# Optimization experiments

Measured on AMD Instinct MI355X. Metric: run time of the kernel, lower is better.

## Reference

```python
import jax, jax.numpy as jnp
import numpy as np
from jax import lax

# ---- config (matches DecodePredictions init kwargs) ----
MAX_PER_CLASS = 100
MAX_TOTAL = 100
IOU_THRESH = 0.5
SCORE_THRESH = 0.05
NUM_CLASSES = 80
K_CAND = 512  # per-class candidate pool kept before NMS (bounds the O(K^2) IoU work)
BOX_VARIANCE = np.array([0.1, 0.1, 0.2, 0.2], np.float32)


def generate_anchors(height, width):
    """RetinaNet anchors (keras.io AnchorBox): FPN levels 3-7, 3 ratios x 3 scales, [cx,cy,w,h] in pixels."""
    ratios = [0.5, 1.0, 2.0]
    scales = [2 ** 0.0, 2 ** (1.0 / 3.0), 2 ** (2.0 / 3.0)]
    all_anchors = []
    for level in range(3, 8):
        stride = 2 ** level
        area = float((2 ** (level + 2)) ** 2)  # 32^2 .. 512^2
        dims = []
        for r in ratios:
            ah = np.sqrt(area / r)
            aw = area / ah
            for s in scales:
                dims.append([s * aw, s * ah])
        dims = np.asarray(dims, np.float32)  # [9, 2] = (w, h)
        fh = int(np.ceil(height / stride))
        fw = int(np.ceil(width / stride))
        rx = (np.arange(fw, dtype=np.float32) + 0.5) * stride
        ry = (np.arange(fh, dtype=np.float32) + 0.5) * stride
        cx, cy = np.meshgrid(rx, ry)
        centers = np.stack([cx, cy], -1)[:, :, None, :].repeat(9, axis=2)  # [fh,fw,9,2]
        d = np.broadcast_to(dims, (fh, fw, 9, 2))
        all_anchors.append(np.concatenate([centers, d], -1).reshape(-1, 4).astype(np.float32))
    return jnp.asarray(np.concatenate(all_anchors, 0))  # [N, 4]


def _pairwise_iou(b):
    # Generic TF NMS IoU formula treating coords as [y1,x1,y2,x2] (module feeds cx,cy,w,h -- replicated faithfully).
    y1, x1, y2, x2 = b[:, 0], b[:, 1], b[:, 2], b[:, 3]
    area = jnp.maximum(y2 - y1, 0.0) * jnp.maximum(x2 - x1, 0.0)
    ih = jnp.maximum(jnp.minimum(y2[:, None], y2[None, :]) - jnp.maximum(y1[:, None], y1[None, :]), 0.0)
    iw = jnp.maximum(jnp.minimum(x2[:, None], x2[None, :]) - jnp.maximum(x1[:, None], x1[None, :]), 0.0)
    inter = ih * iw
    union = area[:, None] + area[None, :] - inter
    return jnp.where(union > 0.0, inter / union, 0.0)


def _nms_single_class(boxes, scores):  # boxes [N,4], scores [N]
    top_s, idx = lax.top_k(scores, K_CAND)          # sort-by-score candidate pool
    top_b = boxes[idx]                               # [K,4]
    keep0 = top_s > SCORE_THRESH                     # score_threshold filter
    iou = _pairwise_iou(top_b)                       # [K,K]
    rng = jnp.arange(K_CAND)

    def body(i, keep):
        sup = (iou[i] > IOU_THRESH) & (rng > i)      # boxes ranked below i suppressed by i
        return jnp.where(keep[i], keep & ~sup, keep)

    keep = lax.fori_loop(0, K_CAND, body, keep0)
    kept_s = jnp.where(keep, top_s, 0.0)
    sel_s, sel = lax.top_k(kept_s, MAX_PER_CLASS)    # max_output_size_per_class
    return top_b[sel], sel_s                         # [P,4], [P]


def _combine(cls_boxes, cls_scores):  # [C,P,4], [C,P] -> combined top MAX_TOTAL for one image
    C, P = cls_scores.shape
    flat_s = cls_scores.reshape(-1)
    flat_b = cls_boxes.reshape(-1, 4)
    flat_c = jnp.repeat(jnp.arange(C, dtype=jnp.float32), P)
    top_s, idx = lax.top_k(flat_s, MAX_TOTAL)
    valid = (top_s > 0.0)
    vf = valid.astype(flat_b.dtype)
    boxes = jnp.clip(flat_b[idx], 0.0, 1.0) * vf[:, None]  # clip_boxes=True, zero-pad invalid
    scores = top_s * vf
    classes = jnp.where(valid, flat_c[idx], 0.0)
    return boxes, scores, classes, valid.sum().astype(jnp.int32)


def _forward(inputs, predictions):
    H, W = inputs.shape[1], inputs.shape[2]
    anchors = generate_anchors(float(H), float(W))            # [N,4] cx,cy,w,h
    cls_scores = jax.nn.sigmoid(predictions[..., :-4])        # [B,N,C]
    box_pred = predictions[..., -4:] * jnp.asarray(BOX_VARIANCE)
    xy = box_pred[..., :2] * anchors[..., 2:] + anchors[..., :2]
    wh = jnp.exp(box_pred[..., 2:]) * anchors[..., 2:]
    boxes = jnp.concatenate([xy, wh], -1)                     # [B,N,4] decoded

    per_class = jax.vmap(jax.vmap(_nms_single_class, in_axes=(None, 1)), in_axes=(0, 0))
    cb, cs = per_class(boxes, cls_scores)                     # [B,C,P,4], [B,C,P]
    return jax.vmap(_combine)(cb, cs)                         # boxes, scores, classes, valid


def setup_inputs() -> dict:
    key = jax.random.key(0)
    k1, k2 = jax.random.split(key)
    inputs = jax.random.uniform(k1, (4, 640, 640, 3), jnp.float32)
    predictions = jax.random.normal(k2, (4, 76725, NUM_CLASSES + 4), jnp.float32)
    return {"inputs": inputs, "predictions": predictions}


def reference(inputs, predictions):
    return _forward(inputs, predictions)
```

## Files before the change

kernel.cpp:

```cpp
#include <hip/hip_runtime.h>
#include <cmath>

#define NA 76725
#define NCLS 80
#define NB 4
#define KC 512
#define MPC 100
#define MT 100
#define TT 256
#define NTILE 300
#define NSLOTP 300
#define PADN 76800
#define NCAND 1024
#define SLOT 16
#define SPLIT 8
#define THRESH_LOGIT 2.3f

struct Dims { float d[5 * 9 * 2]; };


__device__ __forceinline__ unsigned keyof(float x) {
    unsigned u = __float_as_uint(x);
    return u ^ ((u & 0x80000000u) ? 0xFFFFFFFFu : 0x80000000u);
}
__device__ __forceinline__ float unkey(unsigned k) {
    unsigned u = (k & 0x80000000u) ? (k ^ 0x80000000u) : ~k;
    return __uint_as_float(u);
}
__device__ __forceinline__ float sigmoidf_dev(float x) {
    if (x >= 0.f) return 1.f / (1.f + expf(-x));
    float e = expf(x);
    return e / (1.f + e);
}
__device__ __forceinline__ unsigned long long compose(unsigned key, int a) {
    return ((unsigned long long)key << 32) | (unsigned long long)(0xFFFFFFFFu - (unsigned)a);
}

__device__ __forceinline__ float4 decode_box(float4 p, int a, const Dims& dims) {
    const int base[5] = {0, 57600, 72000, 75600, 76500};
    const int fw[5] = {80, 40, 20, 10, 5};
    const float strd[5] = {8.f, 16.f, 32.f, 64.f, 128.f};
    int l;
    if (a < 57600) l = 0;
    else if (a < 72000) l = 1;
    else if (a < 75600) l = 2;
    else if (a < 76500) l = 3;
    else l = 4;
    int i = a - base[l];
    int cell = i / 9, k = i - cell * 9;
    int x = cell % fw[l], y = cell / fw[l];
    float cx = ((float)x + 0.5f) * strd[l];
    float cy = ((float)y + 0.5f) * strd[l];
    float aw = dims.d[(l * 9 + k) * 2 + 0];
    float ah = dims.d[(l * 9 + k) * 2 + 1];
    float bx = __fmul_rn(p.x, 0.1f), by = __fmul_rn(p.y, 0.1f);
    float bw = __fmul_rn(p.z, 0.2f), bh = __fmul_rn(p.w, 0.2f);
    float4 o;
    o.x = __fadd_rn(__fmul_rn(bx, aw), cx);
    o.y = __fadd_rn(__fmul_rn(by, ah), cy);
    o.z = __fmul_rn(expf(bw), aw);
    o.w = __fmul_rn(expf(bh), ah);
    return o;
}


__global__ __launch_bounds__(256) void scan_kernel(const float* __restrict__ pred,
                                                   unsigned long long* __restrict__ candbuf,
                                                   int* __restrict__ counts2) {
    __shared__ int cnt[NCLS];
    __shared__ unsigned long long hitbuf[NCLS * SLOT];
    const int blk = blockIdx.x;
    const int b = blk / NTILE, tix = blk - b * NTILE;
    const int t0 = tix * TT;
    int nrow = NA - t0; if (nrow > TT) nrow = TT;

    if (threadIdx.x < NCLS) cnt[threadIdx.x] = 0;
    __syncthreads();

    const float4* src = reinterpret_cast<const float4*>(pred + ((size_t)b * NA + t0) * 84);
    const int nv = nrow * 21;

    #define PROC(v, idx) do {                                                  \
        const int row_ = (idx) / 21, chunk_ = (idx) - row_ * 21;               \
        if (chunk_ != 20) {                                                    \
            const int a_ = t0 + row_, cbase_ = chunk_ * 4;                     \
            const float vals_[4] = {(v).x, (v).y, (v).z, (v).w};               \
            _Pragma("unroll")                                                  \
            for (int q_ = 0; q_ < 4; ++q_) {                                   \
                if (vals_[q_] > THRESH_LOGIT) {                                \
                    const int c_ = cbase_ + q_;                                \
                    const int p_ = atomicAdd(&cnt[c_], 1);                     \
                    if (p_ < SLOT)                                             \
                        hitbuf[c_ * SLOT + p_] = compose(keyof(vals_[q_]), a_);\
                }                                                              \
            }                                                                  \
        }                                                                      \
    } while (0)

    int i = threadIdx.x;
    for (; i + 768 < nv; i += 1024) {
        const float4 v0 = src[i];
        const float4 v1 = src[i + 256];
        const float4 v2 = src[i + 512];
        const float4 v3 = src[i + 768];
        PROC(v0, i); PROC(v1, i + 256); PROC(v2, i + 512); PROC(v3, i + 768);
    }
    for (; i < nv; i += 256) {
        const float4 v = src[i];
        PROC(v, i);
    }
    #undef PROC
    __syncthreads();

    for (int e = threadIdx.x; e < NCLS * SLOT; e += 256) {
        const int c = e >> 4, q = e & (SLOT - 1);
        if (q < cnt[c])
            candbuf[(((size_t)(b * NCLS + c)) * NSLOTP + tix) * SLOT + q] = hitbuf[e];
    }
    if (threadIdx.x < NCLS)
        counts2[(size_t)(b * NCLS + threadIdx.x) * NSLOTP + tix] = cnt[threadIdx.x];
}


__device__ __forceinline__ void find_bin(int* hist, int bins, int remaining,
                                         int* sh3, int* wsum) {
    const int tid = threadIdx.x;
    const int lane = tid & 63, wv = tid >> 6;
    const int nit = (bins + 511) >> 9;
    int lsum = 0;
    for (int q = 0; q < nit; ++q) {
        int rr = tid * nit + q;
        if (rr < bins) lsum += hist[bins - 1 - rr];
    }
    int acc = lsum;
    #pragma unroll
    for (int off = 1; off < 64; off <<= 1) {
        int x = __shfl_up(acc, off);
        if (lane >= off) acc += x;
    }
    if (lane == 63) wsum[wv] = acc;
    __syncthreads();
    int base = 0;
    for (int w = 0; w < wv; ++w) base += wsum[w];
    int run = base + acc - lsum;
    for (int q = 0; q < nit; ++q) {
        int rr = tid * nit + q;
        if (rr < bins) {
            int h = hist[bins - 1 - rr];
            if (run < remaining && remaining <= run + h) { sh3[0] = bins - 1 - rr; sh3[1] = run; sh3[2] = h; }
            run += h;
        }
    }
    __syncthreads();
}


__global__ __launch_bounds__(512) void topk2_kernel(const float* __restrict__ pred,
                                                    const unsigned long long* __restrict__ candbuf,
                                                    const int* __restrict__ counts2,
                                                    float* __restrict__ top_score,
                                                    float4* __restrict__ sel_boxes, Dims dims) {
    const int col = blockIdx.x;
    const int b = col / NCLS, cc = col - b * NCLS;
    const int tid = threadIdx.x;
    const int lane = tid & 63, wv = tid >> 6;

    __shared__ int hist4k[4096];
    __shared__ unsigned long long buf[KC];
    __shared__ int hist[256];
    __shared__ int sh3[3];
    __shared__ int wsum[8];
    __shared__ int gcount, eqtaken, totsh, ovfsh;
    __shared__ int wcnt[8];
    unsigned long long* cand = (unsigned long long*)hist4k;
    int* scnt = hist4k + 2048;
    int* spfx = hist4k + 2560;

    if (tid == 0) { totsh = 0; ovfsh = 0; }
    int lsum = (tid < NSLOTP) ? counts2[(size_t)col * NSLOTP + tid] : 0;
    scnt[tid] = lsum;
    if (lsum > SLOT) ovfsh = 1;
    int acc = lsum;
    #pragma unroll
    for (int off = 1; off < 64; off <<= 1) {
        int x = __shfl_up(acc, off);
        if (lane >= off) acc += x;
    }
    if (lane == 63) wsum[wv] = acc;
    __syncthreads();
    int base = 0;
    for (int w = 0; w < wv; ++w) base += wsum[w];
    spfx[tid] = base + acc - lsum;
    if (tid == 511) totsh = base + acc;
    __syncthreads();

    const int tot = totsh;
    const bool fastok = (!ovfsh) && tot >= KC && tot <= NCAND;
    int mode = 0;

    if (fastok) {
        cand[tid] = 0ull; cand[tid + 512] = 0ull;
        __syncthreads();
        const unsigned long long* src = candbuf + (size_t)col * NSLOTP * SLOT;
        for (int i = tid; i < NSLOTP * SLOT; i += 512) {
            const int e = i >> 4, q = i & (SLOT - 1);
            const unsigned long long v = src[i];
            if (q < scnt[e]) cand[spfx[e] + q] = v;
        }
        __syncthreads();
    } else {
        const float* colp = pred + (size_t)b * NA * 84 + cc;
        for (int i = tid; i < 4096; i += 512) hist4k[i] = 0;
        __syncthreads();
        for (int a = tid; a < NA; a += 512)
            atomicAdd(&hist4k[keyof(colp[(size_t)a * 84]) >> 20], 1);
        __syncthreads();
        find_bin(hist4k, 4096, KC, sh3, wsum);
        const int bsel = sh3[0], above = sh3[1], ceq1 = sh3[2];
        const int ncand = above + ceq1;

        if (ncand <= NCAND) {
            const unsigned fk = ((unsigned)bsel) << 20;
            if (tid == 0) gcount = 0;
            cand[tid] = 0ull; cand[tid + 512] = 0ull;
            __syncthreads();
            for (int a = tid; a < NA; a += 512) {
                unsigned k = keyof(colp[(size_t)a * 84]);
                if (k >= fk) { int p = atomicAdd(&gcount, 1); cand[p] = compose(k, a); }
            }
            __syncthreads();
        } else {
            mode = 1;
            unsigned prefix = ((unsigned)bsel) << 20;
            int remaining = KC - above;

            for (int i = tid; i < 4096; i += 512) hist4k[i] = 0;
            __syncthreads();
            for (int a = tid; a < NA; a += 512) {
                unsigned k = keyof(colp[(size_t)a * 84]);
                if ((k & 0xFFF00000u) == prefix) atomicAdd(&hist4k[(k >> 8) & 4095], 1);
            }
            __syncthreads();
            find_bin(hist4k, 4096, remaining, sh3, wsum);
            prefix |= ((unsigned)sh3[0]) << 8;
            remaining -= sh3[1];

            if (tid < 256) hist[tid] = 0;
            __syncthreads();
            for (int a = tid; a < NA; a += 512) {
                unsigned k = keyof(colp[(size_t)a * 84]);
                if ((k & 0xFFFFFF00u) == prefix) atomicAdd(&hist[k & 255], 1);
            }
            __syncthreads();
            find_bin(hist, 256, remaining, sh3, wsum);
            prefix |= (unsigned)sh3[0];
            remaining -= sh3[1];

            const unsigned K = prefix;
            const int cgt = KC - remaining;
            const int need = remaining;
            if (tid == 0) { gcount = 0; eqtaken = 0; }
            __syncthreads();
            for (int bs = 0; bs < PADN; bs += 512) {
                int a = bs + tid;
                unsigned key = (a < NA) ? keyof(colp[(size_t)a * 84]) : 0u;
                if (a < NA && key > K) {
                    int p = atomicAdd(&gcount, 1);
                    buf[p] = compose(key, a);
                }
                bool eq = (key == K) && (a < NA);
                unsigned long long m = __ballot(eq);
                if (lane == 0) wcnt[wv] = __popcll(m);
                __syncthreads();
                int off = eqtaken;
                for (int w = 0; w < wv; ++w) off += wcnt[w];
                int rank = off + __popcll(m & ((1ull << lane) - 1ull));
                if (eq && rank < need)
                    buf[cgt + rank] = compose(K, a);
                __syncthreads();
                if (tid == 0) {
                    int s = 0;
                    for (int w = 0; w < 8; ++w) s += wcnt[w];
                    eqtaken += s;
                }
                __syncthreads();
            }
        }
    }

    if (mode == 0) {
        for (int k2 = 2; k2 <= NCAND; k2 <<= 1) {
            for (int j = k2 >> 1; j > 0; j >>= 1) {
                __syncthreads();
                for (int i = tid; i < NCAND; i += 512) {
                    int ixj = i ^ j;
                    if (ixj > i) {
                        unsigned long long A = cand[i], B = cand[ixj];
                        bool up = (i & k2) == 0;
                        if (up ? (A < B) : (A > B)) { cand[i] = B; cand[ixj] = A; }
                    }
                }
            }
        }
    } else {
        for (int k2 = 2; k2 <= KC; k2 <<= 1) {
            for (int j = k2 >> 1; j > 0; j >>= 1) {
                __syncthreads();
                {
                    int i = tid, ixj = i ^ j;
                    if (ixj > i) {
                        unsigned long long A = buf[i], B = buf[ixj];
                        bool up = (i & k2) == 0;
                        if (up ? (A < B) : (A > B)) { buf[i] = B; buf[ixj] = A; }
                    }
                }
            }
        }
    }
    __syncthreads();

    {
        const unsigned long long v = (mode == 0) ? cand[tid] : buf[tid];
        const unsigned key = (unsigned)(v >> 32);
        const int a = (int)(0xFFFFFFFFu - (unsigned)(v & 0xFFFFFFFFu));
        top_score[col * KC + tid] = sigmoidf_dev(unkey(key));
        const float4 p4 = *reinterpret_cast<const float4*>(pred + ((size_t)b * NA + a) * 84 + 80);
        sel_boxes[(size_t)col * KC + tid] = decode_box(p4, a, dims);
    }
}


__global__ __launch_bounds__(512) void nms_build_kernel(const float4* __restrict__ sel_boxes,
                                                        unsigned long long* __restrict__ maskbuf) {
    const int blk = blockIdx.x;
    const int col = blk >> 3, part = blk & 7;
    const int tid = threadIdx.x, wave = tid >> 6, lane = tid & 63;
    __shared__ float y1[KC], x1[KC], y2[KC], x2[KC], ar[KC];

    for (int t = tid; t < KC; t += 512) {
        float4 bx = sel_boxes[(size_t)col * KC + t];
        y1[t] = bx.x; x1[t] = bx.y; y2[t] = bx.z; x2[t] = bx.w;
        ar[t] = __fmul_rn(fmaxf(__fsub_rn(bx.z, bx.x), 0.f),
                          fmaxf(__fsub_rn(bx.w, bx.y), 0.f));
    }
    __syncthreads();

    float jy1[8], jx1[8], jy2[8], jx2[8], jar[8];
    #pragma unroll
    for (int w = 0; w < 8; ++w) {
        int j = (w << 6) + lane;
        jy1[w] = y1[j]; jx1[w] = x1[j]; jy2[w] = y2[j]; jx2[w] = x2[j]; jar[w] = ar[j];
    }

    for (int k = 0; k < 8; ++k) {
        const int i = part + SPLIT * (wave + 8 * k);
        const float iy1 = y1[i], ix1 = x1[i], iy2 = y2[i], ix2 = x2[i], iar = ar[i];
        unsigned long long row[8];
        #pragma unroll
        for (int w = 0; w < 8; ++w) {
            unsigned long long m = 0ull;
            if (((w << 6) + 63) > i) {
                const int j = (w << 6) + lane;
                float ih = fmaxf(__fsub_rn(fminf(iy2, jy2[w]), fmaxf(iy1, jy1[w])), 0.f);
                float iw = fmaxf(__fsub_rn(fminf(ix2, jx2[w]), fmaxf(ix1, jx1[w])), 0.f);
                float inter = __fmul_rn(ih, iw);
                float uni = __fsub_rn(__fadd_rn(iar, jar[w]), inter);
                m = __ballot((uni > 0.f) && (inter > __fmul_rn(0.5f, uni)) && (j > i));
            }
            row[w] = m;
        }
        unsigned long long v = row[0];
        v = (lane == 1) ? row[1] : v;
        v = (lane == 2) ? row[2] : v;
        v = (lane == 3) ? row[3] : v;
        v = (lane == 4) ? row[4] : v;
        v = (lane == 5) ? row[5] : v;
        v = (lane == 6) ? row[6] : v;
        v = (lane == 7) ? row[7] : v;
        if (lane < 8) maskbuf[((size_t)col * KC + i) * 8 + lane] = v;
    }
}


__global__ __launch_bounds__(512) void nms_resolve_kernel(const float4* __restrict__ sel_boxes,
                                                          const float* __restrict__ top_score,
                                                          const unsigned long long* __restrict__ maskbuf,
                                                          float4* __restrict__ col_boxes,
                                                          float* __restrict__ col_scores) {
    const int col = blockIdx.x;
    const int tid = threadIdx.x, wv = tid >> 6, lane = tid & 63;
    __shared__ unsigned long long mask[KC * 8];
    __shared__ float y1[KC], x1[KC], y2[KC], x2[KC], sc[KC];
    __shared__ unsigned long long keep0w[8], keepw[8];
    __shared__ int wordpfx[9];
    __shared__ int sel[MPC];

    {
        const unsigned long long* src = maskbuf + (size_t)col * KC * 8;
        for (int m = tid; m < KC * 8; m += 512) mask[m] = src[m];
    }
    {
        const int t = tid;
        float4 bx = sel_boxes[(size_t)col * KC + t];
        y1[t] = bx.x; x1[t] = bx.y; y2[t] = bx.z; x2[t] = bx.w;
        const float s = top_score[col * KC + t];
        sc[t] = s;
        const unsigned long long m = __ballot(s > 0.05f);
        if (lane == 0) keep0w[t >> 6] = m;
    }
    __syncthreads();

    if (wv == 0) {
        const int w8 = lane & 7;
        const unsigned long long kww = keep0w[w8];
        unsigned long long remw = 0ull;
        for (int ib = 0; ib < KC; ib += 8) {
            unsigned long long rows[8];
            #pragma unroll
            for (int u = 0; u < 8; ++u) rows[u] = mask[(ib + u) * 8 + w8];
            #pragma unroll
            for (int u = 0; u < 8; ++u) {
                const int i = ib + u, W = i >> 6, t = i & 63;
                const unsigned long long remW = __shfl(remw, W);
                const unsigned long long kwW = __shfl(kww, W);
                if (((kwW >> t) & 1ull) && !((remW >> t) & 1ull)) remw |= rows[u];
            }
        }
        if (lane < 8) keepw[w8] = kww & ~remw;
    }
    __syncthreads();
    if (tid == 0) {
        int s = 0;
        #pragma unroll
        for (int w = 0; w < 8; ++w) { wordpfx[w] = s; s += __popcll(keepw[w]); }
        wordpfx[8] = s;
    }
    __syncthreads();

    const int nkept = wordpfx[8];
    {
        const int t = tid;
        const unsigned long long w = keepw[t >> 6];
        const int l = t & 63;
        const bool kp = (w >> l) & 1ull;
        const int kb = wordpfx[t >> 6] + __popcll(w & ((1ull << l) - 1ull));
        if (kp) {
            if (kb < MPC) sel[kb] = t;
        } else {
            const int nb = t - kb;
            if (nkept + nb < MPC) sel[nkept + nb] = t;
        }
    }
    __syncthreads();
    if (tid < MPC) {
        int t = sel[tid];
        bool kp = (keepw[t >> 6] >> (t & 63)) & 1ull;
        col_scores[col * MPC + tid] = kp ? sc[t] : 0.f;
        col_boxes[col * MPC + tid] = make_float4(y1[t], x1[t], y2[t], x2[t]);
    }
}


__global__ __launch_bounds__(1024) void combine_kernel(const float4* __restrict__ col_boxes,
                                                       const float* __restrict__ col_scores,
                                                       float* __restrict__ out) {
    const int b = blockIdx.x, tid = threadIdx.x;
    const int wv = tid >> 6, lane = tid & 63;
    __shared__ int hist[256];
    __shared__ unsigned long long cand[128];
    __shared__ int sh3[3];
    __shared__ int gcnt, eqtaken;
    __shared__ int wcnt[16];
    __shared__ int wsc[16];

    const int NTOT = NCLS * MPC;
    unsigned sck[8];
    #pragma unroll
    for (int q = 0; q < 8; ++q) {
        const int t = (q << 10) + tid;
        sck[q] = (t < NTOT) ? __float_as_uint(col_scores[b * NTOT + t]) : 0u;
    }

    unsigned prefix = 0;
    int remaining = MT, ceq = 0;
    #pragma unroll 1
    for (int pass = 0; pass < 4; ++pass) {
        const int shift = 24 - 8 * pass;
        const unsigned mdone = pass ? (0xFFFFFFFFu << (shift + 8)) : 0u;
        if (tid < 256) hist[tid] = 0;
        __syncthreads();
        #pragma unroll
        for (int q = 0; q < 8; ++q) {
            const int t = (q << 10) + tid;
            if (t < NTOT && (sck[q] & mdone) == prefix)
                atomicAdd(&hist[(sck[q] >> shift) & 255], 1);
        }
        __syncthreads();
        int lsum = (tid < 256) ? hist[255 - tid] : 0;
        int acc2 = lsum;
        #pragma unroll
        for (int off = 1; off < 64; off <<= 1) {
            int x = __shfl_up(acc2, off);
            if (lane >= off) acc2 += x;
        }
        if (lane == 63) wsc[wv] = acc2;
        __syncthreads();
        int base2 = 0;
        for (int w = 0; w < wv; ++w) base2 += wsc[w];
        int run = base2 + acc2 - lsum;
        if (tid < 256 && run < remaining && remaining <= run + lsum) { sh3[0] = 255 - tid; sh3[1] = run; sh3[2] = lsum; }
        __syncthreads();
        prefix |= ((unsigned)sh3[0]) << shift;
        remaining -= sh3[1];
        ceq = sh3[2];
        __syncthreads();
    }
    const unsigned S = prefix;
    const int cgt = MT - remaining;

    if (tid == 0) { gcnt = 0; eqtaken = 0; }
    if (tid < 128) cand[tid] = 0ull;
    __syncthreads();
    #pragma unroll
    for (int q = 0; q < 8; ++q) {
        const int t = (q << 10) + tid;
        if (t < NTOT && sck[q] > S) {
            int p = atomicAdd(&gcnt, 1);
            cand[p] = ((unsigned long long)sck[q] << 32) |
                      (unsigned long long)(0xFFFFFFFFu - (unsigned)t);
        }
    }
    __syncthreads();

    if (ceq == remaining) {
        #pragma unroll
        for (int q = 0; q < 8; ++q) {
            const int t = (q << 10) + tid;
            if (t < NTOT && sck[q] == S) {
                int p = atomicAdd(&eqtaken, 1);
                cand[cgt + p] = ((unsigned long long)S << 32) |
                                (unsigned long long)(0xFFFFFFFFu - (unsigned)t);
            }
        }
        __syncthreads();
    } else {
        #pragma unroll 1
        for (int q = 0; q < 8; ++q) {
            const int t = (q << 10) + tid;
            const bool eq = (t < NTOT) && (sck[q] == S);
            unsigned long long m = __ballot(eq);
            if (lane == 0) wcnt[wv] = __popcll(m);
            __syncthreads();
            int off = eqtaken;
            for (int w = 0; w < wv; ++w) off += wcnt[w];
            int rank = off + __popcll(m & ((1ull << lane) - 1ull));
            if (eq && rank < remaining)
                cand[cgt + rank] = ((unsigned long long)S << 32) |
                                   (unsigned long long)(0xFFFFFFFFu - (unsigned)t);
            __syncthreads();
            if (tid == 0) {
                int s = 0;
                for (int w = 0; w < 16; ++w) s += wcnt[w];
                eqtaken += s;
            }
            __syncthreads();
        }
    }

    for (int k2 = 2; k2 <= 128; k2 <<= 1) {
        for (int j = k2 >> 1; j > 0; j >>= 1) {
            __syncthreads();
            if (tid < 128) {
                int i = tid, ixj = i ^ j;
                if (ixj > i) {
                    unsigned long long A = cand[i], B = cand[ixj];
                    bool up = (i & k2) == 0;
                    if (up ? (A < B) : (A > B)) { cand[i] = B; cand[ixj] = A; }
                }
            }
        }
    }
    __syncthreads();
    if (tid == 0) gcnt = 0;
    __syncthreads();
    if (tid < MT) {
        unsigned long long v = cand[tid];
        float s = __uint_as_float((unsigned)(v >> 32));
        int f = (int)(0xFFFFFFFFu - (unsigned)(v & 0xFFFFFFFFu));
        bool valid = (s > 0.f);
        int cl = 0, p = 0;
        float4 bx = make_float4(0.f, 0.f, 0.f, 0.f);
        if (valid) {
            cl = f / MPC;
            p = f - cl * MPC;
            float4 raw = col_boxes[((size_t)b * NCLS + cl) * MPC + p];
            bx.x = fminf(fmaxf(raw.x, 0.f), 1.f);
            bx.y = fminf(fmaxf(raw.y, 0.f), 1.f);
            bx.z = fminf(fmaxf(raw.z, 0.f), 1.f);
            bx.w = fminf(fmaxf(raw.w, 0.f), 1.f);
            atomicAdd(&gcnt, 1);
        }
        int o = b * MT + tid;
        out[o * 4 + 0] = bx.x;
        out[o * 4 + 1] = bx.y;
        out[o * 4 + 2] = bx.z;
        out[o * 4 + 3] = bx.w;
        out[NB * MT * 4 + o] = valid ? s : 0.f;
        out[NB * MT * 5 + o] = valid ? (float)cl : 0.f;
    }
    __syncthreads();
    if (tid == 0) out[NB * MT * 6 + b] = (float)gcnt;
}


extern "C" void kernel_launch(void* const* d_in, const int* in_sizes, int n_in,
                              void* d_out, int out_size, void* d_ws, size_t ws_size,
                              hipStream_t stream) {
    const float* pred = (const float*)d_in[1];
    float* out = (float*)d_out;
    char* ws = (char*)d_ws;

    Dims dims;
    const double ratios[3] = {0.5, 1.0, 2.0};
    for (int l = 0; l < 5; ++l) {
        double side = (double)(1 << (l + 5));
        double area = side * side;
        for (int ri = 0; ri < 3; ++ri) {
            double ah = sqrt(area / ratios[ri]);
            double aw = area / ah;
            for (int si = 0; si < 3; ++si) {
                double s = pow(2.0, (double)si / 3.0);
                dims.d[(l * 9 + ri * 3 + si) * 2 + 0] = (float)(s * aw);
                dims.d[(l * 9 + ri * 3 + si) * 2 + 1] = (float)(s * ah);
            }
        }
    }

    const size_t SZ_CAND = (size_t)NB * NCLS * NSLOTP * SLOT * 8;
    const size_t SZ_CNT  = (size_t)NB * NCLS * NSLOTP * 4;
    const size_t SZ_SC   = (size_t)NB * NCLS * KC * 4;
    const size_t SZ_SEL  = (size_t)NB * NCLS * KC * 16;
    const size_t SZ_CB   = (size_t)NB * NCLS * MPC * 16;

    unsigned long long* candbuf    = (unsigned long long*)(ws);
    int*                counts2    = (int*)(ws + SZ_CAND);
    float*              top_score  = (float*)(ws + SZ_CAND + SZ_CNT);
    float4*             sel_boxes  = (float4*)(ws + SZ_CAND + SZ_CNT + SZ_SC);
    float4*             col_boxes  = (float4*)(ws + SZ_CAND + SZ_CNT + SZ_SC + SZ_SEL);
    float*              col_scores = (float*)(ws + SZ_CAND + SZ_CNT + SZ_SC + SZ_SEL + SZ_CB);
    unsigned long long* maskbuf    = (unsigned long long*)(ws);

    scan_kernel<<<NB * NTILE, 256, 0, stream>>>(pred, candbuf, counts2);
    topk2_kernel<<<NB * NCLS, 512, 0, stream>>>(pred, candbuf, counts2, top_score, sel_boxes, dims);
    nms_build_kernel<<<NB * NCLS * SPLIT, 512, 0, stream>>>(sel_boxes, maskbuf);
    nms_resolve_kernel<<<NB * NCLS, 512, 0, stream>>>(sel_boxes, top_score, maskbuf, col_boxes, col_scores);
    combine_kernel<<<NB, 1024, 0, stream>>>(col_boxes, col_scores, out);
}
```

Baseline: 297.8 us.

## Fuse five pipeline kernels into one cooperative persistent kernel with grid syncs

Merges the scan, top-k, NMS mask build, NMS resolve and combine stages into a single persistent cooperative kernel, using grid.sync between stages and a shared-memory union across stages. The aim is to remove four kernel launch gaps and inter-kernel drain/fill bubbles. The costs are fewer resident blocks (grid capped at 512) so the heavy scan stage runs with less parallelism, the overhead of grid-wide barriers, and a tail-heavy combine stage that runs on only 4 blocks while the rest idle. The original multi-kernel path is kept as a fallback if the cooperative launch fails.

```diff
diff --git a/kernel.cpp b/kernel.cpp
--- a/kernel.cpp
+++ b/kernel.cpp
@@ -1,4 +1,5 @@
 #include <hip/hip_runtime.h>
+#include <hip/hip_cooperative_groups.h>
 #include <cmath>
 
 #define NA 76725
@@ -63,6 +64,595 @@
     return o;
 }
 
+#define PROC(v, idx) do {                                                  \
+    const int row_ = (idx) / 21, chunk_ = (idx) - row_ * 21;               \
+    if (chunk_ != 20) {                                                    \
+        const int a_ = t0 + row_, cbase_ = chunk_ * 4;                     \
+        const float vals_[4] = {(v).x, (v).y, (v).z, (v).w};               \
+        _Pragma("unroll")                                                  \
+        for (int q_ = 0; q_ < 4; ++q_) {                                   \
+            if (vals_[q_] > THRESH_LOGIT) {                                \
+                const int c_ = cbase_ + q_;                                \
+                const int p_ = atomicAdd(&cnt[c_], 1);                     \
+                if (p_ < SLOT)                                             \
+                    hitbuf[c_ * SLOT + p_] = compose(keyof(vals_[q_]), a_);\
+            }                                                              \
+        }                                                                  \
+    }                                                                      \
+} while (0)
+
+
+__device__ __forceinline__ void find_bin(int* hist, int bins, int remaining,
+                                         int* sh3, int* wsum) {
+    const int tid = threadIdx.x;
+    const int lane = tid & 63, wv = tid >> 6;
+    const int nit = (bins + 511) >> 9;
+    int lsum = 0;
+    for (int q = 0; q < nit; ++q) {
+        int rr = tid * nit + q;
+        if (rr < bins) lsum += hist[bins - 1 - rr];
+    }
+    int acc = lsum;
+    #pragma unroll
+    for (int off = 1; off < 64; off <<= 1) {
+        int x = __shfl_up(acc, off);
+        if (lane >= off) acc += x;
+    }
+    if (lane == 63) wsum[wv] = acc;
+    __syncthreads();
+    int base = 0;
+    for (int w = 0; w < wv; ++w) base += wsum[w];
+    int run = base + acc - lsum;
+    for (int q = 0; q < nit; ++q) {
+        int rr = tid * nit + q;
+        if (rr < bins) {
+            int h = hist[bins - 1 - rr];
+            if (run < remaining && remaining <= run + h) { sh3[0] = bins - 1 - rr; sh3[1] = run; sh3[2] = h; }
+            run += h;
+        }
+    }
+    __syncthreads();
+}
+
+
+struct SScan {
+    int cnt[NCLS];
+    unsigned long long hitbuf[NCLS * SLOT];
+};
+struct STopk {
+    int hist4k[4096];
+    unsigned long long buf[KC];
+    int hist[256];
+    int sh3[3];
+    int wsum[8];
+    int gcount, eqtaken, totsh, ovfsh;
+    int wcnt[8];
+};
+struct SBuild {
+    float y1[KC], x1[KC], y2[KC], x2[KC], ar[KC];
+};
+struct SResolve {
+    unsigned long long mask[KC * 8];
+    float y1[KC], x1[KC], y2[KC], x2[KC], sc[KC];
+    unsigned long long keep0w[8], keepw[8];
+    int wordpfx[9];
+    int sel[MPC];
+};
+struct SComb {
+    int hist[256];
+    unsigned long long cand[128];
+    int sh3[3];
+    int gcnt, eqtaken;
+    int wcnt[8];
+    int wsc[8];
+};
+union SMem {
+    SScan s; STopk t; SBuild b; SResolve r; SComb c;
+};
+
+__global__ __launch_bounds__(512, 4) void mega_kernel(const float* __restrict__ pred,
+                                                      unsigned long long* __restrict__ candbuf,
+                                                      int* __restrict__ counts2,
+                                                      float* __restrict__ top_score,
+                                                      float4* __restrict__ sel_boxes,
+                                                      unsigned long long* __restrict__ maskbuf,
+                                                      float4* __restrict__ col_boxes,
+                                                      float* __restrict__ col_scores,
+                                                      float* __restrict__ out, Dims dims) {
+    __shared__ SMem U;
+    const int tid = threadIdx.x;
+    const int lane = tid & 63, wv = tid >> 6;
+    cooperative_groups::grid_group grid = cooperative_groups::this_grid();
+
+    {
+        int* cnt = U.s.cnt;
+        unsigned long long* hitbuf = U.s.hitbuf;
+        for (int item = blockIdx.x; item < NB * NTILE; item += gridDim.x) {
+            __syncthreads();
+            const int b = item / NTILE, tix = item - b * NTILE;
+            const int t0 = tix * TT;
+            int nrow = NA - t0; if (nrow > TT) nrow = TT;
+            if (tid < NCLS) cnt[tid] = 0;
+            __syncthreads();
+            const float4* src = reinterpret_cast<const float4*>(pred + ((size_t)b * NA + t0) * 84);
+            const int nv = nrow * 21;
+            int i = tid;
+            for (; i + 1536 < nv; i += 2048) {
+                const float4 v0 = src[i];
+                const float4 v1 = src[i + 512];
+                const float4 v2 = src[i + 1024];
+                const float4 v3 = src[i + 1536];
+                PROC(v0, i); PROC(v1, i + 512); PROC(v2, i + 1024); PROC(v3, i + 1536);
+            }
+            for (; i < nv; i += 512) {
+                const float4 v = src[i];
+                PROC(v, i);
+            }
+            __syncthreads();
+            for (int e = tid; e < NCLS * SLOT; e += 512) {
+                const int c = e >> 4, q = e & (SLOT - 1);
+                if (q < cnt[c])
+                    candbuf[(((size_t)(b * NCLS + c)) * NSLOTP + tix) * SLOT + q] = hitbuf[e];
+            }
+            if (tid < NCLS)
+                counts2[(size_t)(b * NCLS + tid) * NSLOTP + tix] = cnt[tid];
+        }
+    }
+    grid.sync();
+
+    {
+        int* hist4k = U.t.hist4k;
+        unsigned long long* buf = U.t.buf;
+        int* hist = U.t.hist;
+        int* sh3 = U.t.sh3;
+        int* wsum = U.t.wsum;
+        int* wcnt = U.t.wcnt;
+        int& gcount = U.t.gcount; int& eqtaken = U.t.eqtaken;
+        int& totsh = U.t.totsh; int& ovfsh = U.t.ovfsh;
+        unsigned long long* cand = (unsigned long long*)hist4k;
+        int* scnt = hist4k + 2048;
+        int* spfx = hist4k + 2560;
+
+        for (int col = blockIdx.x; col < NB * NCLS; col += gridDim.x) {
+            __syncthreads();
+            const int b = col / NCLS, cc = col - b * NCLS;
+
+            if (tid == 0) { totsh = 0; ovfsh = 0; }
+            int lsum = (tid < NSLOTP) ? counts2[(size_t)col * NSLOTP + tid] : 0;
+            scnt[tid] = lsum;
+            if (lsum > SLOT) ovfsh = 1;
+            int acc = lsum;
+            #pragma unroll
+            for (int off = 1; off < 64; off <<= 1) {
+                int x = __shfl_up(acc, off);
+                if (lane >= off) acc += x;
+            }
+            if (lane == 63) wsum[wv] = acc;
+            __syncthreads();
+            int base = 0;
+            for (int w = 0; w < wv; ++w) base += wsum[w];
+            spfx[tid] = base + acc - lsum;
+            if (tid == 511) totsh = base + acc;
+            __syncthreads();
+
+            const int tot = totsh;
+            const bool fastok = (!ovfsh) && tot >= KC && tot <= NCAND;
+            int mode = 0;
+
+            if (fastok) {
+                cand[tid] = 0ull; cand[tid + 512] = 0ull;
+                __syncthreads();
+                const unsigned long long* src = candbuf + (size_t)col * NSLOTP * SLOT;
+                for (int i = tid; i < NSLOTP * SLOT; i += 512) {
+                    const int e = i >> 4, q = i & (SLOT - 1);
+                    const unsigned long long v = src[i];
+                    if (q < scnt[e]) cand[spfx[e] + q] = v;
+                }
+                __syncthreads();
+            } else {
+                const float* colp = pred + (size_t)b * NA * 84 + cc;
+                for (int i = tid; i < 4096; i += 512) hist4k[i] = 0;
+                __syncthreads();
+                for (int a = tid; a < NA; a += 512)
+                    atomicAdd(&hist4k[keyof(colp[(size_t)a * 84]) >> 20], 1);
+                __syncthreads();
+                find_bin(hist4k, 4096, KC, sh3, wsum);
+                const int bsel = sh3[0], above = sh3[1], ceq1 = sh3[2];
+                const int ncand = above + ceq1;
+
+                if (ncand <= NCAND) {
+                    const unsigned fk = ((unsigned)bsel) << 20;
+                    if (tid == 0) gcount = 0;
+                    cand[tid] = 0ull; cand[tid + 512] = 0ull;
+                    __syncthreads();
+                    for (int a = tid; a < NA; a += 512) {
+                        unsigned k = keyof(colp[(size_t)a * 84]);
+                        if (k >= fk) { int p = atomicAdd(&gcount, 1); cand[p] = compose(k, a); }
+                    }
+                    __syncthreads();
+                } else {
+                    mode = 1;
+                    unsigned prefix = ((unsigned)bsel) << 20;
+                    int remaining = KC - above;
+
+                    for (int i = tid; i < 4096; i += 512) hist4k[i] = 0;
+                    __syncthreads();
+                    for (int a = tid; a < NA; a += 512) {
+                        unsigned k = keyof(colp[(size_t)a * 84]);
+                        if ((k & 0xFFF00000u) == prefix) atomicAdd(&hist4k[(k >> 8) & 4095], 1);
+                    }
+                    __syncthreads();
+                    find_bin(hist4k, 4096, remaining, sh3, wsum);
+                    prefix |= ((unsigned)sh3[0]) << 8;
+                    remaining -= sh3[1];
+
+                    if (tid < 256) hist[tid] = 0;
+                    __syncthreads();
+                    for (int a = tid; a < NA; a += 512) {
+                        unsigned k = keyof(colp[(size_t)a * 84]);
+                        if ((k & 0xFFFFFF00u) == prefix) atomicAdd(&hist[k & 255], 1);
+                    }
+                    __syncthreads();
+                    find_bin(hist, 256, remaining, sh3, wsum);
+                    prefix |= (unsigned)sh3[0];
+                    remaining -= sh3[1];
+
+                    const unsigned K = prefix;
+                    const int cgt = KC - remaining;
+                    const int need = remaining;
+                    if (tid == 0) { gcount = 0; eqtaken = 0; }
+                    __syncthreads();
+                    for (int bs = 0; bs < PADN; bs += 512) {
+                        int a = bs + tid;
+                        unsigned key = (a < NA) ? keyof(colp[(size_t)a * 84]) : 0u;
+                        if (a < NA && key > K) {
+                            int p = atomicAdd(&gcount, 1);
+                            buf[p] = compose(key, a);
+                        }
+                        bool eq = (key == K) && (a < NA);
+                        unsigned long long m = __ballot(eq);
+                        if (lane == 0) wcnt[wv] = __popcll(m);
+                        __syncthreads();
+                        int off = eqtaken;
+                        for (int w = 0; w < wv; ++w) off += wcnt[w];
+                        int rank = off + __popcll(m & ((1ull << lane) - 1ull));
+                        if (eq && rank < need)
+                            buf[cgt + rank] = compose(K, a);
+                        __syncthreads();
+                        if (tid == 0) {
+                            int s = 0;
+                            for (int w = 0; w < 8; ++w) s += wcnt[w];
+                            eqtaken += s;
+                        }
+                        __syncthreads();
+                    }
+                }
+            }
+
+            if (mode == 0) {
+                for (int k2 = 2; k2 <= NCAND; k2 <<= 1) {
+                    for (int j = k2 >> 1; j > 0; j >>= 1) {
+                        __syncthreads();
+                        for (int i = tid; i < NCAND; i += 512) {
+                            int ixj = i ^ j;
+                            if (ixj > i) {
+                                unsigned long long A = cand[i], B = cand[ixj];
+                                bool up = (i & k2) == 0;
+                                if (up ? (A < B) : (A > B)) { cand[i] = B; cand[ixj] = A; }
+                            }
+                        }
+                    }
+                }
+            } else {
+                for (int k2 = 2; k2 <= KC; k2 <<= 1) {
+                    for (int j = k2 >> 1; j > 0; j >>= 1) {
+                        __syncthreads();
+                        {
+                            int i = tid, ixj = i ^ j;
+                            if (ixj > i) {
+                                unsigned long long A = buf[i], B = buf[ixj];
+                                bool up = (i & k2) == 0;
+                                if (up ? (A < B) : (A > B)) { buf[i] = B; buf[ixj] = A; }
+                            }
+                        }
+                    }
+                }
+            }
+            __syncthreads();
+
+            {
+                const unsigned long long v = (mode == 0) ? cand[tid] : buf[tid];
+                const unsigned key = (unsigned)(v >> 32);
+                const int a = (int)(0xFFFFFFFFu - (unsigned)(v & 0xFFFFFFFFu));
+                top_score[col * KC + tid] = sigmoidf_dev(unkey(key));
+                const float4 p4 = *reinterpret_cast<const float4*>(pred + ((size_t)b * NA + a) * 84 + 80);
+                sel_boxes[(size_t)col * KC + tid] = decode_box(p4, a, dims);
+            }
+        }
+    }
+    grid.sync();
+
+    {
+        float* y1 = U.b.y1; float* x1 = U.b.x1; float* y2 = U.b.y2;
+        float* x2 = U.b.x2; float* ar = U.b.ar;
+        for (int item = blockIdx.x; item < NB * NCLS * SPLIT; item += gridDim.x) {
+            __syncthreads();
+            const int col = item >> 3, part = item & 7;
+            for (int t = tid; t < KC; t += 512) {
+                float4 bx = sel_boxes[(size_t)col * KC + t];
+                y1[t] = bx.x; x1[t] = bx.y; y2[t] = bx.z; x2[t] = bx.w;
+                ar[t] = __fmul_rn(fmaxf(__fsub_rn(bx.z, bx.x), 0.f),
+                                  fmaxf(__fsub_rn(bx.w, bx.y), 0.f));
+            }
+            __syncthreads();
+
+            float jy1[8], jx1[8], jy2[8], jx2[8], jar[8];
+            #pragma unroll
+            for (int w = 0; w < 8; ++w) {
+                int j = (w << 6) + lane;
+                jy1[w] = y1[j]; jx1[w] = x1[j]; jy2[w] = y2[j]; jx2[w] = x2[j]; jar[w] = ar[j];
+            }
+
+            for (int k = 0; k < 8; ++k) {
+                const int i = part + SPLIT * (wv + 8 * k);
+                const float iy1 = y1[i], ix1 = x1[i], iy2 = y2[i], ix2 = x2[i], iar = ar[i];
+                unsigned long long row[8];
+                #pragma unroll
+                for (int w = 0; w < 8; ++w) {
+                    unsigned long long m = 0ull;
+                    if (((w << 6) + 63) > i) {
+                        const int j = (w << 6) + lane;
+                        float ih = fmaxf(__fsub_rn(fminf(iy2, jy2[w]), fmaxf(iy1, jy1[w])), 0.f);
+                        float iw = fmaxf(__fsub_rn(fminf(ix2, jx2[w]), fmaxf(ix1, jx1[w])), 0.f);
+                        float inter = __fmul_rn(ih, iw);
+                        float uni = __fsub_rn(__fadd_rn(iar, jar[w]), inter);
+                        m = __ballot((uni > 0.f) && (inter > __fmul_rn(0.5f, uni)) && (j > i));
+                    }
+                    row[w] = m;
+                }
+                unsigned long long v = row[0];
+                v = (lane == 1) ? row[1] : v;
+                v = (lane == 2) ? row[2] : v;
+                v = (lane == 3) ? row[3] : v;
+                v = (lane == 4) ? row[4] : v;
+                v = (lane == 5) ? row[5] : v;
+                v = (lane == 6) ? row[6] : v;
+                v = (lane == 7) ? row[7] : v;
+                if (lane < 8) maskbuf[((size_t)col * KC + i) * 8 + lane] = v;
+            }
+        }
+    }
+    grid.sync();
+
+    {
+        unsigned long long* mask = U.r.mask;
+        float* y1 = U.r.y1; float* x1 = U.r.x1; float* y2 = U.r.y2;
+        float* x2 = U.r.x2; float* sc = U.r.sc;
+        unsigned long long* keep0w = U.r.keep0w;
+        unsigned long long* keepw = U.r.keepw;
+        int* wordpfx = U.r.wordpfx;
+        int* sel = U.r.sel;
+
+        for (int col = blockIdx.x; col < NB * NCLS; col += gridDim.x) {
+            __syncthreads();
+            {
+                const unsigned long long* src = maskbuf + (size_t)col * KC * 8;
+                for (int m = tid; m < KC * 8; m += 512) mask[m] = src[m];
+            }
+            {
+                const int t = tid;
+                float4 bx = sel_boxes[(size_t)col * KC + t];
+                y1[t] = bx.x; x1[t] = bx.y; y2[t] = bx.z; x2[t] = bx.w;
+                const float s = top_score[col * KC + t];
+                sc[t] = s;
+                const unsigned long long m = __ballot(s > 0.05f);
+                if (lane == 0) keep0w[t >> 6] = m;
+            }
+            __syncthreads();
+
+            if (wv == 0) {
+                const int w8 = lane & 7;
+                const unsigned long long kww = keep0w[w8];
+                unsigned long long remw = 0ull;
+                for (int ib = 0; ib < KC; ib += 8) {
+                    unsigned long long rows[8];
+                    #pragma unroll
+                    for (int u = 0; u < 8; ++u) rows[u] = mask[(ib + u) * 8 + w8];
+                    #pragma unroll
+                    for (int u = 0; u < 8; ++u) {
+                        const int i = ib + u, W = i >> 6, t = i & 63;
+                        const unsigned long long remW = __shfl(remw, W);
+                        const unsigned long long kwW = __shfl(kww, W);
+                        if (((kwW >> t) & 1ull) && !((remW >> t) & 1ull)) remw |= rows[u];
+                    }
+                }
+                if (lane < 8) keepw[w8] = kww & ~remw;
+            }
+            __syncthreads();
+            if (tid == 0) {
+                int s = 0;
+                #pragma unroll
+                for (int w = 0; w < 8; ++w) { wordpfx[w] = s; s += __popcll(keepw[w]); }
+                wordpfx[8] = s;
+            }
+            __syncthreads();
+
+            const int nkept = wordpfx[8];
+            {
+                const int t = tid;
+                const unsigned long long w = keepw[t >> 6];
+                const int l = t & 63;
+                const bool kp = (w >> l) & 1ull;
+                const int kb = wordpfx[t >> 6] + __popcll(w & ((1ull << l) - 1ull));
+                if (kp) {
+                    if (kb < MPC) sel[kb] = t;
+                } else {
+                    const int nb = t - kb;
+                    if (nkept + nb < MPC) sel[nkept + nb] = t;
+                }
+            }
+            __syncthreads();
+            if (tid < MPC) {
+                int t = sel[tid];
+                bool kp = (keepw[t >> 6] >> (t & 63)) & 1ull;
+                col_scores[col * MPC + tid] = kp ? sc[t] : 0.f;
+                col_boxes[col * MPC + tid] = make_float4(y1[t], x1[t], y2[t], x2[t]);
+            }
+        }
+    }
+    grid.sync();
+
+    {
+        int* hist = U.c.hist;
+        unsigned long long* cand = U.c.cand;
+        int* sh3 = U.c.sh3;
+        int* wcnt = U.c.wcnt;
+        int* wsc = U.c.wsc;
+        int& gcnt = U.c.gcnt; int& eqtaken = U.c.eqtaken;
+        const int NTOT = NCLS * MPC;
+
+        for (int bb = blockIdx.x; bb < NB; bb += gridDim.x) {
+            __syncthreads();
+            unsigned sck[16];
+            #pragma unroll
+            for (int q = 0; q < 16; ++q) {
+                const int t = (q << 9) + tid;
+                sck[q] = (t < NTOT) ? __float_as_uint(col_scores[bb * NTOT + t]) : 0u;
+            }
+
+            unsigned prefix = 0;
+            int remaining = MT, ceq = 0;
+            #pragma unroll 1
+            for (int pass = 0; pass < 4; ++pass) {
+                const int shift = 24 - 8 * pass;
+                const unsigned mdone = pass ? (0xFFFFFFFFu << (shift + 8)) : 0u;
+                if (tid < 256) hist[tid] = 0;
+                __syncthreads();
+                #pragma unroll
+                for (int q = 0; q < 16; ++q) {
+                    const int t = (q << 9) + tid;
+                    if (t < NTOT && (sck[q] & mdone) == prefix)
+                        atomicAdd(&hist[(sck[q] >> shift) & 255], 1);
+                }
+                __syncthreads();
+                int lsum = (tid < 256) ? hist[255 - tid] : 0;
+                int acc2 = lsum;
+                #pragma unroll
+                for (int off = 1; off < 64; off <<= 1) {
+                    int x = __shfl_up(acc2, off);
+                    if (lane >= off) acc2 += x;
+                }
+                if (lane == 63) wsc[wv] = acc2;
+                __syncthreads();
+                int base2 = 0;
+                for (int w = 0; w < wv; ++w) base2 += wsc[w];
+                int run = base2 + acc2 - lsum;
+                if (tid < 256 && run < remaining && remaining <= run + lsum) { sh3[0] = 255 - tid; sh3[1] = run; sh3[2] = lsum; }
+                __syncthreads();
+                prefix |= ((unsigned)sh3[0]) << shift;
+                remaining -= sh3[1];
+                ceq = sh3[2];
+                __syncthreads();
+            }
+            const unsigned S = prefix;
+            const int cgt = MT - remaining;
+
+            if (tid == 0) { gcnt = 0; eqtaken = 0; }
+            if (tid < 128) cand[tid] = 0ull;
+            __syncthreads();
+            #pragma unroll
+            for (int q = 0; q < 16; ++q) {
+                const int t = (q << 9) + tid;
+                if (t < NTOT && sck[q] > S) {
+                    int p = atomicAdd(&gcnt, 1);
+                    cand[p] = ((unsigned long long)sck[q] << 32) |
+                              (unsigned long long)(0xFFFFFFFFu - (unsigned)t);
+                }
+            }
+            __syncthreads();
+
+            if (ceq == remaining) {
+                #pragma unroll
+                for (int q = 0; q < 16; ++q) {
+                    const int t = (q << 9) + tid;
+                    if (t < NTOT && sck[q] == S) {
+                        int p = atomicAdd(&eqtaken, 1);
+                        cand[cgt + p] = ((unsigned long long)S << 32) |
+                                        (unsigned long long)(0xFFFFFFFFu - (unsigned)t);
+                    }
+                }
+                __syncthreads();
+            } else {
+                #pragma unroll 1
+                for (int q = 0; q < 16; ++q) {
+                    const int t = (q << 9) + tid;
+                    const bool eq = (t < NTOT) && (sck[q] == S);
+                    unsigned long long m = __ballot(eq);
+                    if (lane == 0) wcnt[wv] = __popcll(m);
+                    __syncthreads();
+                    int off = eqtaken;
+                    for (int w = 0; w < wv; ++w) off += wcnt[w];
+                    int rank = off + __popcll(m & ((1ull << lane) - 1ull));
+                    if (eq && rank < remaining)
+                        cand[cgt + rank] = ((unsigned long long)S << 32) |
+                                           (unsigned long long)(0xFFFFFFFFu - (unsigned)t);
+                    __syncthreads();
+                    if (tid == 0) {
+                        int s = 0;
+                        for (int w = 0; w < 8; ++w) s += wcnt[w];
+                        eqtaken += s;
+                    }
+                    __syncthreads();
+                }
+            }
+
+            for (int k2 = 2; k2 <= 128; k2 <<= 1) {
+                for (int j = k2 >> 1; j > 0; j >>= 1) {
+                    __syncthreads();
+                    if (tid < 128) {
+                        int i = tid, ixj = i ^ j;
+                        if (ixj > i) {
+                            unsigned long long A = cand[i], B = cand[ixj];
+                            bool up = (i & k2) == 0;
+                            if (up ? (A < B) : (A > B)) { cand[i] = B; cand[ixj] = A; }
+                        }
+                    }
+                }
+            }
+            __syncthreads();
+            if (tid == 0) gcnt = 0;
+            __syncthreads();
+            if (tid < MT) {
+                unsigned long long v = cand[tid];
+                float s = __uint_as_float((unsigned)(v >> 32));
+                int f = (int)(0xFFFFFFFFu - (unsigned)(v & 0xFFFFFFFFu));
+                bool valid = (s > 0.f);
+                int cl = 0, p = 0;
+                float4 bx = make_float4(0.f, 0.f, 0.f, 0.f);
+                if (valid) {
+                    cl = f / MPC;
+                    p = f - cl * MPC;
+                    float4 raw = col_boxes[((size_t)bb * NCLS + cl) * MPC + p];
+                    bx.x = fminf(fmaxf(raw.x, 0.f), 1.f);
+                    bx.y = fminf(fmaxf(raw.y, 0.f), 1.f);
+                    bx.z = fminf(fmaxf(raw.z, 0.f), 1.f);
+                    bx.w = fminf(fmaxf(raw.w, 0.f), 1.f);
+                    atomicAdd(&gcnt, 1);
+                }
+                int o = bb * MT + tid;
+                out[o * 4 + 0] = bx.x;
+                out[o * 4 + 1] = bx.y;
+                out[o * 4 + 2] = bx.z;
+                out[o * 4 + 3] = bx.w;
+                out[NB * MT * 4 + o] = valid ? s : 0.f;
+                out[NB * MT * 5 + o] = valid ? (float)cl : 0.f;
+            }
+            __syncthreads();
+            if (tid == 0) out[NB * MT * 6 + bb] = (float)gcnt;
+        }
+    }
+}
+
 
 __global__ __launch_bounds__(256) void scan_kernel(const float* __restrict__ pred,
                                                    unsigned long long* __restrict__ candbuf,
@@ -80,23 +670,6 @@
     const float4* src = reinterpret_cast<const float4*>(pred + ((size_t)b * NA + t0) * 84);
     const int nv = nrow * 21;
 
-    #define PROC(v, idx) do {                                                  \
-        const int row_ = (idx) / 21, chunk_ = (idx) - row_ * 21;               \
-        if (chunk_ != 20) {                                                    \
-            const int a_ = t0 + row_, cbase_ = chunk_ * 4;                     \
-            const float vals_[4] = {(v).x, (v).y, (v).z, (v).w};               \
-            _Pragma("unroll")                                                  \
-            for (int q_ = 0; q_ < 4; ++q_) {                                   \
-                if (vals_[q_] > THRESH_LOGIT) {                                \
-                    const int c_ = cbase_ + q_;                                \
-                    const int p_ = atomicAdd(&cnt[c_], 1);                     \
-                    if (p_ < SLOT)                                             \
-                        hitbuf[c_ * SLOT + p_] = compose(keyof(vals_[q_]), a_);\
-                }                                                              \
-            }                                                                  \
-        }                                                                      \
-    } while (0)
-
     int i = threadIdx.x;
     for (; i + 768 < nv; i += 1024) {
         const float4 v0 = src[i];
@@ -109,7 +682,6 @@
         const float4 v = src[i];
         PROC(v, i);
     }
-    #undef PROC
     __syncthreads();
 
     for (int e = threadIdx.x; e < NCLS * SLOT; e += 256) {
@@ -120,40 +692,6 @@
     if (threadIdx.x < NCLS)
         counts2[(size_t)(b * NCLS + threadIdx.x) * NSLOTP + tix] = cnt[threadIdx.x];
 }
-
-
-__device__ __forceinline__ void find_bin(int* hist, int bins, int remaining,
-                                         int* sh3, int* wsum) {
-    const int tid = threadIdx.x;
-    const int lane = tid & 63, wv = tid >> 6;
-    const int nit = (bins + 511) >> 9;
-    int lsum = 0;
-    for (int q = 0; q < nit; ++q) {
-        int rr = tid * nit + q;
-        if (rr < bins) lsum += hist[bins - 1 - rr];
-    }
-    int acc = lsum;
-    #pragma unroll
-    for (int off = 1; off < 64; off <<= 1) {
-        int x = __shfl_up(acc, off);
-        if (lane >= off) acc += x;
-    }
-    if (lane == 63) wsum[wv] = acc;
-    __syncthreads();
-    int base = 0;
-    for (int w = 0; w < wv; ++w) base += wsum[w];
-    int run = base + acc - lsum;
-    for (int q = 0; q < nit; ++q) {
-        int rr = tid * nit + q;
-        if (rr < bins) {
-            int h = hist[bins - 1 - rr];
-            if (run < remaining && remaining <= run + h) { sh3[0] = bins - 1 - rr; sh3[1] = run; sh3[2] = h; }
-            run += h;
-        }
-    }
-    __syncthreads();
-}
-
 
 __global__ __launch_bounds__(512) void topk2_kernel(const float* __restrict__ pred,
                                                     const unsigned long long* __restrict__ candbuf,
@@ -328,7 +866,6 @@
         sel_boxes[(size_t)col * KC + tid] = decode_box(p4, a, dims);
     }
 }
-
 
 __global__ __launch_bounds__(512) void nms_build_kernel(const float4* __restrict__ sel_boxes,
                                                         unsigned long long* __restrict__ maskbuf) {
@@ -381,7 +918,6 @@
     }
 }
 
-
 __global__ __launch_bounds__(512) void nms_resolve_kernel(const float4* __restrict__ sel_boxes,
                                                           const float* __restrict__ top_score,
                                                           const unsigned long long* __restrict__ maskbuf,
@@ -459,7 +995,6 @@
         col_boxes[col * MPC + tid] = make_float4(y1[t], x1[t], y2[t], x2[t]);
     }
 }
-
 
 __global__ __launch_bounds__(1024) void combine_kernel(const float4* __restrict__ col_boxes,
                                                        const float* __restrict__ col_scores,
@@ -650,9 +1185,31 @@
     float*              col_scores = (float*)(ws + SZ_CAND + SZ_CNT + SZ_SC + SZ_SEL + SZ_CB);
     unsigned long long* maskbuf    = (unsigned long long*)(ws);
 
-    scan_kernel<<<NB * NTILE, 256, 0, stream>>>(pred, candbuf, counts2);
-    topk2_kernel<<<NB * NCLS, 512, 0, stream>>>(pred, candbuf, counts2, top_score, sel_boxes, dims);
-    nms_build_kernel<<<NB * NCLS * SPLIT, 512, 0, stream>>>(sel_boxes, maskbuf);
-    nms_resolve_kernel<<<NB * NCLS, 512, 0, stream>>>(sel_boxes, top_score, maskbuf, col_boxes, col_scores);
-    combine_kernel<<<NB, 1024, 0, stream>>>(col_boxes, col_scores, out);
+    bool done = false;
+    int mb = 0;
+    hipError_t oe = hipOccupancyMaxActiveBlocksPerMultiprocessor(&mb, mega_kernel, 512, 0);
+    if (oe == hipSuccess && mb >= 1) {
+        int grid = mb * 256;
+        if (grid > 512) grid = 512;
+        if (grid >= 8) {
+            void* kargs[] = {(void*)&pred, (void*)&candbuf, (void*)&counts2,
+                             (void*)&top_score, (void*)&sel_boxes, (void*)&maskbuf,
+                             (void*)&col_boxes, (void*)&col_scores, (void*)&out,
+                             (void*)&dims};
+            hipError_t le = hipLaunchCooperativeKernel(reinterpret_cast<void*>(mega_kernel),
+                                                       dim3(grid), dim3(512), kargs, 0, stream);
+            if (le == hipSuccess) done = true;
+            else (void)hipGetLastError();
+        }
+    } else {
+        (void)hipGetLastError();
+    }
+
+    if (!done) {
+        scan_kernel<<<NB * NTILE, 256, 0, stream>>>(pred, candbuf, counts2);
+        topk2_kernel<<<NB * NCLS, 512, 0, stream>>>(pred, candbuf, counts2, top_score, sel_boxes, dims);
+        nms_build_kernel<<<NB * NCLS * SPLIT, 512, 0, stream>>>(sel_boxes, maskbuf);
+        nms_resolve_kernel<<<NB * NCLS, 512, 0, stream>>>(sel_boxes, top_score, maskbuf, col_boxes, col_scores);
+        combine_kernel<<<NB, 1024, 0, stream>>>(col_boxes, col_scores, out);
+    }
 }
```

Result: slower. 509.5 us (+71.1%).
